# Kernel optimization log

Measured on AMD Instinct MI355X. Metric: run time of the kernel, lower is better.

## Reference

```python
import jax, jax.numpy as jnp
import numpy as np

B = 512

def conv2d(x, w, b, stride, pad):
    y = jax.lax.conv_general_dilated(x, w, (stride, stride), [(pad, pad), (pad, pad)],
                                     dimension_numbers=('NCHW', 'OIHW', 'NCHW'))
    return y + b[None, :, None, None]

def maxpool(x, k, s, pad):
    return jax.lax.reduce_window(x, -jnp.inf, jax.lax.max,
                                 (1, 1, k, k), (1, 1, s, s),
                                 [(0, 0), (0, 0), (pad, pad), (pad, pad)])

def squash(s, axis=-1):
    sq = jnp.sum(s * s, axis=axis, keepdims=True)
    return (sq / (1.0 + sq)) * s / jnp.sqrt(sq + 1e-8)

def setup_inputs() -> dict:
    key = jax.random.key(0)
    ks = jax.random.split(key, 24)
    def w(k, shape, fan_in):
        return jax.random.normal(k, shape, dtype=jnp.float32) * np.float32(np.sqrt(2.0 / fan_in))
    inp = {}
    inp['x']  = jax.random.normal(ks[0], (B, 1, 28, 28), dtype=jnp.float32)
    inp['w1'] = w(ks[1], (96, 1, 3, 3), 1 * 9);     inp['b1'] = jnp.zeros((96,), jnp.float32)
    inp['w2'] = w(ks[2], (256, 96, 3, 3), 96 * 9);  inp['b2'] = jnp.zeros((256,), jnp.float32)
    inp['w3'] = w(ks[3], (384, 256, 3, 3), 256 * 9);inp['b3'] = jnp.zeros((384,), jnp.float32)
    inp['w4'] = w(ks[4], (384, 384, 3, 3), 384 * 9);inp['b4'] = jnp.zeros((384,), jnp.float32)
    inp['w5'] = w(ks[5], (256, 384, 3, 3), 384 * 9);inp['b5'] = jnp.zeros((256,), jnp.float32)
    # PrimaryCaps conv: 256 -> 32 caps * 8 dim = 256 channels, k2 s1 p0
    inp['wp'] = w(ks[6], (256, 256, 2, 2), 256 * 4);inp['bp'] = jnp.zeros((256,), jnp.float32)
    # DenseCapsule routing weight [out_caps=10, in_caps=512, out_dim=16, in_dim=8]
    inp['Wr'] = jax.random.normal(ks[7], (10, 512, 16, 8), dtype=jnp.float32) * 0.01
    inp['fw1'] = w(ks[8], (4096, 160), 160);   inp['fb1'] = jnp.zeros((4096,), jnp.float32)
    inp['fw2'] = w(ks[9], (4096, 4096), 4096); inp['fb2'] = jnp.zeros((4096,), jnp.float32)
    inp['fw3'] = w(ks[10], (10, 4096), 4096);  inp['fb3'] = jnp.zeros((10,), jnp.float32)
    return inp

def reference(x, w1, b1, w2, b2, w3, b3, w4, b4, w5, b5, wp, bp, Wr,
              fw1, fb1, fw2, fb2, fw3, fb3):
    # AlexNet-style conv stack (eval mode; dropout = identity)
    h = jax.nn.relu(conv2d(x, w1, b1, 1, 1))   # [B,96,28,28]
    h = maxpool(h, 3, 2, 1)                    # [B,96,14,14]
    h = jax.nn.relu(conv2d(h, w2, b2, 1, 1))   # [B,256,14,14]
    h = maxpool(h, 3, 2, 1)                    # [B,256,7,7]
    h = jax.nn.relu(conv2d(h, w3, b3, 1, 1))   # [B,384,7,7]
    h = jax.nn.relu(conv2d(h, w4, b4, 1, 1))   # [B,384,7,7]
    h = jax.nn.relu(conv2d(h, w5, b5, 1, 1))   # [B,256,7,7]
    h = maxpool(h, 3, 1, 0)                    # [B,256,5,5]
    # PrimaryCaps: conv k2 -> [B,256,4,4] -> [B,512,8] -> squash
    p = conv2d(h, wp, bp, 1, 0)                # [B,256,4,4]
    u = p.reshape(p.shape[0], -1, 8)           # [B,512,8]
    u = squash(u)
    # DenseCapsule dynamic routing (3 iterations)
    x_hat = jnp.einsum('oivd,bid->boiv', Wr, u)     # [B,10,512,16]
    x_hat_d = jax.lax.stop_gradient(x_hat)
    b = jnp.zeros(x_hat.shape[:3], x_hat.dtype)     # [B,10,512]
    routings = 3
    for i in range(routings):
        c = jax.nn.softmax(b, axis=1)
        if i == routings - 1:
            v = squash(jnp.einsum('boi,boiv->bov', c, x_hat))
        else:
            v = squash(jnp.einsum('boi,boiv->bov', c, x_hat_d))
            b = b + jnp.einsum('bov,boiv->boi', v, x_hat_d)
    # Flatten + FC head
    f = v.reshape(v.shape[0], -1)                   # [B,160]
    f = jax.nn.relu(f @ fw1.T + fb1)
    f = jax.nn.relu(f @ fw2.T + fb2)
    return f @ fw3.T + fb3                          # [B,10]
```

## Files before the change

### kernel.cpp

```cpp
#include <hip/hip_runtime.h>
#include <math.h>


#define BATCH 512

typedef _Float16 half8  __attribute__((ext_vector_type(8)));
typedef _Float16 half4v __attribute__((ext_vector_type(4)));
typedef float   float4v __attribute__((ext_vector_type(4)));

__device__ __forceinline__ void gload_lds16(const void* g, void* l)
{
    __builtin_amdgcn_global_load_lds(
        (const __attribute__((address_space(1))) unsigned int*)g,
        (__attribute__((address_space(3))) unsigned int*)l,
        16, 0, 0);
}

__global__ __launch_bounds__(64) void zero_kernel(float* __restrict__ z)
{
    z[threadIdx.x] = 0.f;
}

__global__ __launch_bounds__(256) void split_kernel(
    const float* __restrict__ src, _Float16* __restrict__ hi,
    _Float16* __restrict__ lo, int n)
{
    int idx = blockIdx.x * 256 + threadIdx.x;
    if (idx >= n) return;
    float v = src[idx];
    _Float16 h = (_Float16)v;
    hi[idx] = h;
    lo[idx] = (_Float16)((v - (float)h) * 2048.0f);
}

__global__ __launch_bounds__(256) void wsplit_pad_kernel(
    const float* __restrict__ src, _Float16* __restrict__ hi,
    _Float16* __restrict__ lo, int IC, int KK, int K, int KP, int total)
{
    int idx = blockIdx.x * 256 + threadIdx.x;
    if (idx >= total) return;
    int k  = idx % KP;
    int oc = idx / KP;
    float v = 0.f;
    if (k < K) {
        int khkw = k / IC;
        int ic   = k - khkw * IC;
        v = src[((size_t)(oc * IC + ic)) * KK + khkw];
    }
    _Float16 h = (_Float16)v;
    hi[idx] = h;
    lo[idx] = (_Float16)((v - (float)h) * 2048.0f);
}

__global__ __launch_bounds__(256) void conv1_pool_nhwc(
    const float* __restrict__ x, const float* __restrict__ w1,
    const float* __restrict__ b1, _Float16* __restrict__ oh_,
    _Float16* __restrict__ ol_)
{
    int idx = blockIdx.x * 256 + threadIdx.x;
    if (idx >= 512 * 14 * 14 * 96) return;
    int oc = idx % 96; int t1 = idx / 96;
    int ow = t1 % 14;  int t2 = t1 / 14;
    int oh = t2 % 14;  int n  = t2 / 14;
    const float* xi = x + n * 784;
    float w[9];
#pragma unroll
    for (int i = 0; i < 9; ++i) w[i] = w1[oc * 9 + i];
    float bias = b1[oc];
    float best = -3.4e38f;
#pragma unroll
    for (int dy = 0; dy < 3; ++dy) {
        int ph = oh * 2 - 1 + dy;
        if ((unsigned)ph >= 28u) continue;
#pragma unroll
        for (int dx = 0; dx < 3; ++dx) {
            int pw = ow * 2 - 1 + dx;
            if ((unsigned)pw >= 28u) continue;
            float s = bias;
#pragma unroll
            for (int ky = 0; ky < 3; ++ky) {
                int iy = ph - 1 + ky;
                if ((unsigned)iy >= 28u) continue;
#pragma unroll
                for (int kx = 0; kx < 3; ++kx) {
                    int ix = pw - 1 + kx;
                    if ((unsigned)ix >= 28u) continue;
                    s = fmaf(w[ky * 3 + kx], xi[iy * 28 + ix], s);
                }
            }
            s = fmaxf(s, 0.f);
            best = fmaxf(best, s);
        }
    }
    _Float16 h = (_Float16)best;
    oh_[idx] = h;
    ol_[idx] = (_Float16)((best - (float)h) * 2048.0f);
}

template<int NB, int C, int H, int W, int OH, int OW, int KS, int STR, int PADP>
__global__ __launch_bounds__(256) void maxpool_nhwc_split(
    const float* __restrict__ in, _Float16* __restrict__ po,
    _Float16* __restrict__ pl)
{
    constexpr int TOTAL = NB * OH * OW * C;
    int idx = blockIdx.x * 256 + threadIdx.x;
    if (idx >= TOTAL) return;
    int c  = idx % C;  int t1 = idx / C;
    int ow = t1 % OW;  int t2 = t1 / OW;
    int oh = t2 % OH;  int n  = t2 / OH;
    const float* ip = in + (size_t)n * (H * W * C) + c;
    float best = -3.4e38f;
#pragma unroll
    for (int dy = 0; dy < KS; ++dy) {
        int ih = oh * STR - PADP + dy;
        if ((unsigned)ih >= (unsigned)H) continue;
#pragma unroll
        for (int dx = 0; dx < KS; ++dx) {
            int iw = ow * STR - PADP + dx;
            if ((unsigned)iw >= (unsigned)W) continue;
            best = fmaxf(best, ip[(size_t)(ih * W + iw) * C]);
        }
    }
    _Float16 h = (_Float16)best;
    po[idx] = h;
    pl[idx] = (_Float16)((best - (float)h) * 2048.0f);
}

template<int IC, int H, int W, int KH, int PAD, int OC, int NT, int OUTMODE>
__global__ __launch_bounds__(256, 2) void conv_dma(
    const _Float16* __restrict__ inh, const _Float16* __restrict__ inl,
    const _Float16* __restrict__ whi, const _Float16* __restrict__ wlo,
    const float* __restrict__ bias, const float* __restrict__ zpage,
    float* __restrict__ outf, _Float16* __restrict__ outh,
    _Float16* __restrict__ outl, int n_base)
{
    constexpr int OH  = H + 2 * PAD - KH + 1;
    constexpr int OW  = W + 2 * PAD - KH + 1;
    constexpr int OHW = OH * OW;
    constexpr int K   = IC * KH * KH;
    constexpr int KP  = (K + 63) & ~63;
    constexpr int NFRAG = NT / 32;
    constexpr int NBI   = NT / 32;
    constexpr bool UNIF = (IC % 64 == 0) && (KP == K);
    constexpr int HWIC = H * W * IC;

    const int t    = threadIdx.x;
    const int lane = t & 63;
    const int wid  = t >> 6;
    const int l15  = lane & 15;
    const int quad = lane >> 4;
    const int wm   = (wid >> 1) << 6;
    const int wn   = (wid & 1) * (NT / 2);

    const int drow  = lane >> 3;
    const int pslot = lane & 7;
    const int slog  = pslot ^ drow;

    __shared__ __align__(16) _Float16 Ah[128 * 64];
    __shared__ __align__(16) _Float16 Al[128 * 64];
    __shared__ __align__(16) _Float16 Bh[NT * 64];
    __shared__ __align__(16) _Float16 Bl[NT * 64];

    const int n0 = blockIdx.x * NT;
    const int m0 = blockIdx.y << 7;

    float4v acc1[4 * NFRAG], acc2[4 * NFRAG];
#pragma unroll
    for (int i = 0; i < 4 * NFRAG; ++i) {
        acc1[i] = (float4v)(0.f);
        acc2[i] = (float4v)(0.f);
    }

    int bU[NBI], ohU[NBI], owU[NBI];
#pragma unroll
    for (int ii = 0; ii < NBI; ++ii) {
        int nl = ((wid * NBI + ii) << 3) + drow;
        int gn = n_base + n0 + nl;
        int b  = gn / OHW;
        int p  = gn - b * OHW;
        int o  = p / OW;
        bU[ii] = b; ohU[ii] = o; owU[ii] = p - o * OW;
    }

    int khkw = 0, icb = 0;
    for (int kb = 0; kb < KP; kb += 64) {
#pragma unroll
        for (int ii = 0; ii < 4; ++ii) {
            const int iA = (wid << 2) + ii;
            const size_t go = (size_t)(m0 + (iA << 3) + drow) * KP + kb + (slog << 3);
            gload_lds16(whi + go, &Ah[(size_t)iA << 9]);
            gload_lds16(wlo + go, &Al[(size_t)iA << 9]);
        }
        if constexpr (UNIF) {
            const int kh = khkw / KH;
            const int kw = khkw - kh * KH;
#pragma unroll
            for (int ii = 0; ii < NBI; ++ii) {
                const int iB = wid * NBI + ii;
                const int ih = ohU[ii] + kh - PAD;
                const int iw = owU[ii] + kw - PAD;
                const bool ok = ((unsigned)ih < (unsigned)H) && ((unsigned)iw < (unsigned)W);
                const size_t off = (size_t)bU[ii] * HWIC + (ih * W + iw) * IC + icb + (slog << 3);
                const _Float16* sh = ok ? inh + off : (const _Float16*)zpage;
                const _Float16* sl = ok ? inl + off : (const _Float16*)zpage;
                gload_lds16(sh, &Bh[(size_t)iB << 9]);
                gload_lds16(sl, &Bl[(size_t)iB << 9]);
            }
            icb += 64;
            if (icb == IC) { icb = 0; ++khkw; }
        } else {
            const int kpl = kb + (slog << 3);
            const int kkl = kpl / IC;
            const int icl = kpl - kkl * IC;
            const int khl = kkl / KH;
            const int kwl = kkl - khl * KH;
#pragma unroll
            for (int ii = 0; ii < NBI; ++ii) {
                const int iB = wid * NBI + ii;
                const int ih = ohU[ii] + khl - PAD;
                const int iw = owU[ii] + kwl - PAD;
                const bool ok = (kpl < K) && ((unsigned)ih < (unsigned)H) &&
                                ((unsigned)iw < (unsigned)W);
                const size_t off = (size_t)bU[ii] * HWIC + (ih * W + iw) * IC + icl;
                const _Float16* sh = ok ? inh + off : (const _Float16*)zpage;
                const _Float16* sl = ok ? inl + off : (const _Float16*)zpage;
                gload_lds16(sh, &Bh[(size_t)iB << 9]);
                gload_lds16(sl, &Bl[(size_t)iB << 9]);
            }
        }
        __syncthreads();
#pragma unroll
        for (int kh2 = 0; kh2 < 2; ++kh2) {
            half8 a_h[4], a_l[4], b_h[NFRAG], b_l[NFRAG];
#pragma unroll
            for (int i = 0; i < 4; ++i) {
                const int r  = wm + (i << 4) + l15;
                const int sl = ((kh2 << 2) + quad) ^ (r & 7);
                const int off = (r << 6) + (sl << 3);
                a_h[i] = *(const half8*)&Ah[off];
                a_l[i] = *(const half8*)&Al[off];
            }
#pragma unroll
            for (int i = 0; i < NFRAG; ++i) {
                const int r  = wn + (i << 4) + l15;
                const int sl = ((kh2 << 2) + quad) ^ (r & 7);
                const int off = (r << 6) + (sl << 3);
                b_h[i] = *(const half8*)&Bh[off];
                b_l[i] = *(const half8*)&Bl[off];
            }
#pragma unroll
            for (int mi = 0; mi < 4; ++mi)
#pragma unroll
                for (int ni = 0; ni < NFRAG; ++ni) {
                    const int ix = mi * NFRAG + ni;
                    acc1[ix] = __builtin_amdgcn_mfma_f32_16x16x32_f16(a_h[mi], b_h[ni], acc1[ix], 0, 0, 0);
                    acc2[ix] = __builtin_amdgcn_mfma_f32_16x16x32_f16(a_h[mi], b_l[ni], acc2[ix], 0, 0, 0);
                    acc2[ix] = __builtin_amdgcn_mfma_f32_16x16x32_f16(a_l[mi], b_h[ni], acc2[ix], 0, 0, 0);
                }
        }
        __syncthreads();
    }
#pragma unroll
    for (int mi = 0; mi < 4; ++mi)
#pragma unroll
        for (int ni = 0; ni < NFRAG; ++ni) {
            const int ix = mi * NFRAG + ni;
            const int gn = n_base + n0 + wn + (ni << 4) + l15;
            const int ln = gn - n_base;
            const int mb = m0 + wm + (mi << 4) + (quad << 2);
            float4v bv = *(const float4v*)(bias + mb);
            float vv[4];
#pragma unroll
            for (int r = 0; r < 4; ++r) {
                float v = acc1[ix][r] + acc2[ix][r] * (1.0f / 2048.0f) + bv[r];
                if (OUTMODE != 2) v = fmaxf(v, 0.f);
                vv[r] = v;
            }
            if (OUTMODE == 0) {
                float4v o = {vv[0], vv[1], vv[2], vv[3]};
                *(float4v*)(outf + (size_t)ln * OC + mb) = o;
            } else if (OUTMODE == 1) {
                half4v hh, ll;
#pragma unroll
                for (int r = 0; r < 4; ++r) {
                    _Float16 h = (_Float16)vv[r];
                    hh[r] = h;
                    ll[r] = (_Float16)((vv[r] - (float)h) * 2048.0f);
                }
                *(half4v*)(outh + (size_t)ln * OC + mb) = hh;
                *(half4v*)(outl + (size_t)ln * OC + mb) = ll;
            } else {
                int b = gn / OHW;
                int p = gn - b * OHW;
#pragma unroll
                for (int r = 0; r < 4; ++r)
                    outf[((size_t)b * OC + mb + r) * OHW + p] = vv[r];
            }
        }
}

__global__ __launch_bounds__(256, 2) void fc2_dma(
    const _Float16* __restrict__ ah_g, const _Float16* __restrict__ al_g,
    const _Float16* __restrict__ bh_g, const _Float16* __restrict__ bl_g,
    float* __restrict__ part, int kslice)
{
    constexpr int K = 4096, N = 4096;
    const int t    = threadIdx.x;
    const int lane = t & 63;
    const int wid  = t >> 6;
    const int l15  = lane & 15;
    const int quad = lane >> 4;
    const int wm   = (wid >> 1) << 6;
    const int wn   = (wid & 1) << 6;

    const int drow  = lane >> 3;
    const int pslot = lane & 7;
    const int slog  = pslot ^ drow;

    __shared__ __align__(16) _Float16 Ah[128 * 64];
    __shared__ __align__(16) _Float16 Al[128 * 64];
    __shared__ __align__(16) _Float16 Bh[128 * 64];
    __shared__ __align__(16) _Float16 Bl[128 * 64];

    const int n0 = blockIdx.x << 7;
    const int m0 = blockIdx.y << 7;
    const int kbeg = blockIdx.z * kslice;

    float4v acc1[16], acc2[16];
#pragma unroll
    for (int i = 0; i < 16; ++i) {
        acc1[i] = (float4v)(0.f);
        acc2[i] = (float4v)(0.f);
    }

    for (int kb = 0; kb < kslice; kb += 64) {
#pragma unroll
        for (int ii = 0; ii < 4; ++ii) {
            const int iA = (wid << 2) + ii;
            const size_t ga = (size_t)(m0 + (iA << 3) + drow) * K + kbeg + kb + (slog << 3);
            gload_lds16(ah_g + ga, &Ah[(size_t)iA << 9]);
            gload_lds16(al_g + ga, &Al[(size_t)iA << 9]);
            const size_t gb = (size_t)(n0 + (iA << 3) + drow) * K + kbeg + kb + (slog << 3);
            gload_lds16(bh_g + gb, &Bh[(size_t)iA << 9]);
            gload_lds16(bl_g + gb, &Bl[(size_t)iA << 9]);
        }
        __syncthreads();
#pragma unroll
        for (int kh2 = 0; kh2 < 2; ++kh2) {
            half8 a_h[4], a_l[4], b_h[4], b_l[4];
#pragma unroll
            for (int i = 0; i < 4; ++i) {
                const int ra  = wm + (i << 4) + l15;
                const int sa  = ((kh2 << 2) + quad) ^ (ra & 7);
                const int oa  = (ra << 6) + (sa << 3);
                a_h[i] = *(const half8*)&Ah[oa];
                a_l[i] = *(const half8*)&Al[oa];
                const int rb  = wn + (i << 4) + l15;
                const int sb  = ((kh2 << 2) + quad) ^ (rb & 7);
                const int ob  = (rb << 6) + (sb << 3);
                b_h[i] = *(const half8*)&Bh[ob];
                b_l[i] = *(const half8*)&Bl[ob];
            }
#pragma unroll
            for (int mi = 0; mi < 4; ++mi)
#pragma unroll
                for (int ni = 0; ni < 4; ++ni) {
                    const int ix = mi * 4 + ni;
                    acc1[ix] = __builtin_amdgcn_mfma_f32_16x16x32_f16(a_h[mi], b_h[ni], acc1[ix], 0, 0, 0);
                    acc2[ix] = __builtin_amdgcn_mfma_f32_16x16x32_f16(a_h[mi], b_l[ni], acc2[ix], 0, 0, 0);
                    acc2[ix] = __builtin_amdgcn_mfma_f32_16x16x32_f16(a_l[mi], b_h[ni], acc2[ix], 0, 0, 0);
                }
        }
        __syncthreads();
    }
    float* po = part + (size_t)blockIdx.z * (512 * 4096);
#pragma unroll
    for (int mi = 0; mi < 4; ++mi)
#pragma unroll
        for (int ni = 0; ni < 4; ++ni) {
            const int ix = mi * 4 + ni;
            const int gn = n0 + wn + (ni << 4) + l15;
#pragma unroll
            for (int r = 0; r < 4; ++r) {
                const int m = m0 + wm + (mi << 4) + (quad << 2) + r;
                po[(size_t)m * N + gn] = acc1[ix][r] + acc2[ix][r] * (1.0f / 2048.0f);
            }
        }
}

__global__ __launch_bounds__(256) void fc2_reduce_kernel(
    const float* __restrict__ part, const float* __restrict__ bias,
    float* __restrict__ out)
{
    int idx = blockIdx.x * 256 + threadIdx.x;
    if (idx >= 512 * 4096) return;
    const size_t MN = (size_t)512 * 4096;
    float s = 0.f;
#pragma unroll
    for (int zz = 0; zz < 4; ++zz) s += part[zz * MN + idx];
    s += bias[idx & 4095];
    out[idx] = fmaxf(s, 0.f);
}

template<bool RELU>
__global__ __launch_bounds__(256) void fc_gemm(
    const float* __restrict__ A, const float* __restrict__ Bw,
    const float* __restrict__ bias, float* __restrict__ out,
    int K, int N)
{
    const int t  = threadIdx.x;
    const int j0 = blockIdx.x << 6;
    const int m0 = blockIdx.y << 7;

    __shared__ __align__(16) float As[16 * 132];
    __shared__ __align__(16) float Bs[16 * 64];

    float acc[8][4];
#pragma unroll
    for (int a = 0; a < 8; ++a)
#pragma unroll
        for (int b = 0; b < 4; ++b) acc[a][b] = 0.f;

    const int a_m  = t >> 2;
    const int a_k  = (t & 3) << 2;
    const int b_j  = t & 63;
    const int b_k0 = (t >> 6) << 2;
    const int ms = (t >> 4) << 3;
    const int js = (t & 15) << 2;

    for (int kb0 = 0; kb0 < K; kb0 += 16) {
#pragma unroll
        for (int r = 0; r < 2; ++r) {
            int m = m0 + a_m + (r << 6);
            float4 av = *(const float4*)(A + (size_t)m * K + kb0 + a_k);
            As[(a_k + 0) * 132 + a_m + (r << 6)] = av.x;
            As[(a_k + 1) * 132 + a_m + (r << 6)] = av.y;
            As[(a_k + 2) * 132 + a_m + (r << 6)] = av.z;
            As[(a_k + 3) * 132 + a_m + (r << 6)] = av.w;
        }
        {
            float4 bv = *(const float4*)(Bw + (size_t)(j0 + b_j) * K + kb0 + b_k0);
            Bs[(b_k0 + 0) * 64 + b_j] = bv.x;
            Bs[(b_k0 + 1) * 64 + b_j] = bv.y;
            Bs[(b_k0 + 2) * 64 + b_j] = bv.z;
            Bs[(b_k0 + 3) * 64 + b_j] = bv.w;
        }
        __syncthreads();
#pragma unroll
        for (int kk = 0; kk < 16; ++kk) {
            float4 A0 = *(const float4*)&As[kk * 132 + ms];
            float4 A1 = *(const float4*)&As[kk * 132 + ms + 4];
            float4 B0 = *(const float4*)&Bs[(kk << 6) + js];
            float av[8] = {A0.x, A0.y, A0.z, A0.w, A1.x, A1.y, A1.z, A1.w};
            float bv[4] = {B0.x, B0.y, B0.z, B0.w};
#pragma unroll
            for (int mm = 0; mm < 8; ++mm)
#pragma unroll
                for (int jj = 0; jj < 4; ++jj)
                    acc[mm][jj] = fmaf(av[mm], bv[jj], acc[mm][jj]);
        }
        __syncthreads();
    }
    float4 b4 = *(const float4*)(bias + j0 + js);
// ... 156 lines not shown
                    acc = fmaf(v_s[(o << 4) + v], xp[(size_t)v * (256 * 512)], acc);
                b_s[p] = acc;
            }
            __syncthreads();
        }
    }

    for (int idx = t; idx < 160; idx += 256) vout[(size_t)b * 160 + idx] = v_s[idx];
}

__global__ __launch_bounds__(256) void fc3_kernel(
    const float* __restrict__ f, const float* __restrict__ w,
    const float* __restrict__ bias, float* __restrict__ out)
{
    const int n = blockIdx.x;
    const int t = threadIdx.x;
    const int lane = t & 63, wv = t >> 6;
    const float* fr = f + (size_t)n * 4096;
    float p[10];
#pragma unroll
    for (int j = 0; j < 10; ++j) p[j] = 0.f;
    for (int k = t; k < 4096; k += 256) {
        float x = fr[k];
#pragma unroll
        for (int j = 0; j < 10; ++j) p[j] = fmaf(x, w[j * 4096 + k], p[j]);
    }
    __shared__ float red[4 * 10];
#pragma unroll
    for (int j = 0; j < 10; ++j) {
        float x = p[j];
        for (int off = 32; off > 0; off >>= 1) x += __shfl_xor(x, off);
        p[j] = x;
    }
    if (lane == 0) {
#pragma unroll
        for (int j = 0; j < 10; ++j) red[wv * 10 + j] = p[j];
    }
    __syncthreads();
    if (t < 10)
        out[(size_t)n * 10 + t] = red[t] + red[10 + t] + red[20 + t] + red[30 + t] + bias[t];
}

extern "C" void kernel_launch(void* const* d_in, const int* in_sizes, int n_in,
                              void* d_out, int out_size, void* d_ws, size_t ws_size,
                              hipStream_t stream)
{
    const float* x   = (const float*)d_in[0];
    const float* w1  = (const float*)d_in[1];
    const float* b1  = (const float*)d_in[2];
    const float* w2  = (const float*)d_in[3];
    const float* b2  = (const float*)d_in[4];
    const float* w3  = (const float*)d_in[5];
    const float* b3  = (const float*)d_in[6];
    const float* w4  = (const float*)d_in[7];
    const float* b4  = (const float*)d_in[8];
    const float* w5  = (const float*)d_in[9];
    const float* b5  = (const float*)d_in[10];
    const float* wp  = (const float*)d_in[11];
    const float* bp  = (const float*)d_in[12];
    const float* Wr  = (const float*)d_in[13];
    const float* fw1 = (const float*)d_in[14];
    const float* fb1 = (const float*)d_in[15];
    const float* fw2 = (const float*)d_in[16];
    const float* fb2 = (const float*)d_in[17];
    const float* fw3 = (const float*)d_in[18];
    const float* fb3 = (const float*)d_in[19];
    float* outp = (float*)d_out;

    char* w = (char*)d_ws;
    _Float16* w2h  = (_Float16*)(w + 115605504);
    _Float16* w2l  = (_Float16*)(w + 116064256);
    _Float16* w3h  = (_Float16*)(w + 116523008);
    _Float16* w3l  = (_Float16*)(w + 118292480);
    _Float16* w4h  = (_Float16*)(w + 120061952);
    _Float16* w4l  = (_Float16*)(w + 122716160);
    _Float16* w5h  = (_Float16*)(w + 125370368);
    _Float16* w5l  = (_Float16*)(w + 127139840);
    _Float16* wph  = (_Float16*)(w + 128909312);
    _Float16* wpl  = (_Float16*)(w + 129433600);
    float*    zp   = (float*)(w + 129957888);

    _Float16* p1h  = (_Float16*)(w + 0);
    _Float16* p1l  = (_Float16*)(w + 19267584);
    float*    a2   = (float*)(w + 38535168);
    _Float16* p2h  = (_Float16*)(w + 89915392);
    _Float16* p2l  = (_Float16*)(w + 102760448);
    _Float16* a3h  = (_Float16*)(w + 0);
    _Float16* a3l  = (_Float16*)(w + 19267584);
    _Float16* a4h  = (_Float16*)(w + 38535168);
    _Float16* a4l  = (_Float16*)(w + 57802752);
    float*    a5   = (float*)(w + 0);
    _Float16* p3h  = (_Float16*)(w + 25690112);
    _Float16* p3l  = (_Float16*)(w + 32243712);
    float*    pc   = (float*)(w + 0);
    float*    u    = (float*)(w + 8388608);
    float*    vcap = (float*)(w + 16777216);
    float*    xh   = (float*)(w + 17104896);

    float*    f1   = (float*)(w + 17104896);
    _Float16* fw2h = (_Float16*)(w + 33882112);
    _Float16* fw2l = (_Float16*)(w + 67436544);
    _Float16* f1h  = (_Float16*)(w + 100990976);
    _Float16* f1l  = (_Float16*)(w + 105185280);
    float*    part = (float*)(w + 0);
    float*    f2   = (float*)(w + 33882112);

    zero_kernel<<<dim3(1), dim3(64), 0, stream>>>(zp);
    wsplit_pad_kernel<<<dim3(896),  dim3(256), 0, stream>>>(w2, w2h, w2l,  96, 9,  864,  896,  229376);
    wsplit_pad_kernel<<<dim3(3456), dim3(256), 0, stream>>>(w3, w3h, w3l, 256, 9, 2304, 2304,  884736);
    wsplit_pad_kernel<<<dim3(5184), dim3(256), 0, stream>>>(w4, w4h, w4l, 384, 9, 3456, 3456, 1327104);
    wsplit_pad_kernel<<<dim3(3456), dim3(256), 0, stream>>>(w5, w5h, w5l, 384, 9, 3456, 3456,  884736);
    wsplit_pad_kernel<<<dim3(1024), dim3(256), 0, stream>>>(wp, wph, wpl, 256, 4, 1024, 1024,  262144);

    conv1_pool_nhwc<<<dim3(37632), dim3(256), 0, stream>>>(x, w1, b1, p1h, p1l);

    conv_dma<96, 14, 14, 3, 1, 256, 128, 0><<<dim3(392, 2), dim3(256), 0, stream>>>(
        p1h, p1l, w2h, w2l, b2, zp, a2, nullptr, nullptr, 0);
    maxpool_nhwc_split<256, 256, 14, 14, 7, 7, 3, 2, 1><<<dim3(12544), dim3(256), 0, stream>>>(
        a2, p2h, p2l);
    conv_dma<96, 14, 14, 3, 1, 256, 128, 0><<<dim3(392, 2), dim3(256), 0, stream>>>(
        p1h, p1l, w2h, w2l, b2, zp, a2, nullptr, nullptr, 50176);
    maxpool_nhwc_split<256, 256, 14, 14, 7, 7, 3, 2, 1><<<dim3(12544), dim3(256), 0, stream>>>(
        a2, p2h + (size_t)3211264, p2l + (size_t)3211264);

    conv_dma<256, 7, 7, 3, 1, 384, 128, 1><<<dim3(196, 3), dim3(256), 0, stream>>>(
        p2h, p2l, w3h, w3l, b3, zp, nullptr, a3h, a3l, 0);
    conv_dma<384, 7, 7, 3, 1, 384, 128, 1><<<dim3(196, 3), dim3(256), 0, stream>>>(
        a3h, a3l, w4h, w4l, b4, zp, nullptr, a4h, a4l, 0);
    conv_dma<384, 7, 7, 3, 1, 256, 128, 0><<<dim3(196, 2), dim3(256), 0, stream>>>(
        a4h, a4l, w5h, w5l, b5, zp, a5, nullptr, nullptr, 0);
    maxpool_nhwc_split<512, 256, 7, 7, 5, 5, 3, 1, 0><<<dim3(12800), dim3(256), 0, stream>>>(
        a5, p3h, p3l);
    conv_dma<256, 5, 5, 2, 0, 256, 64, 2><<<dim3(128, 2), dim3(256), 0, stream>>>(
        p3h, p3l, wph, wpl, bp, zp, pc, nullptr, nullptr, 0);
    squash_kernel<<<dim3(1024), dim3(256), 0, stream>>>(pc, u);

    for (int h = 0; h < 2; ++h) {
        const float* uh = u + (size_t)h * 256 * 4096;
        float* vh = vcap + (size_t)h * 256 * 160;
        xhat_kernel<<<dim3(16, 10), dim3(256), 0, stream>>>(uh, Wr, xh);
        routing2_kernel<<<dim3(256), dim3(256), 0, stream>>>(xh, vh);
    }

    split_kernel<<<dim3(65536), dim3(256), 0, stream>>>(fw2, fw2h, fw2l, 16777216);

    fc_gemm<true><<<dim3(64, 4), dim3(256), 0, stream>>>(vcap, fw1, fb1, f1, 160, 4096);
    split_kernel<<<dim3(8192), dim3(256), 0, stream>>>(f1, f1h, f1l, 2097152);
    fc2_dma<<<dim3(32, 4, 4), dim3(256), 0, stream>>>(f1h, f1l, fw2h, fw2l, part, 1024);
    fc2_reduce_kernel<<<dim3(8192), dim3(256), 0, stream>>>(part, fb2, f2);
    fc3_kernel<<<dim3(512), dim3(256), 0, stream>>>(f2, fw3, fb3, outp);
}
```

Measured before the change: 1.403 ms.

## Double-buffer LDS in conv and FC2 GEMMs with 8-wave blocks

Rewrites the conv and FC2 GEMM kernels so they double-buffer the LDS tiles. The next K-slice's global-to-LDS DMA loads are issued before computing on the current slice, gated by explicit vmcnt waits and raw s_barrier. Blocks grow from 4 to 8 waves, with per-wave N work halved, and MFMA sections are bracketed with s_setprio. The goal is to overlap memory latency with MFMA work. The cost is doubled LDS per block, which likely allows only one block per CU and reduces scheduling flexibility.

```diff
diff --git a/kernel.cpp b/kernel.cpp
--- a/kernel.cpp
+++ b/kernel.cpp
@@ -14,6 +14,14 @@
         (const __attribute__((address_space(1))) unsigned int*)g,
         (__attribute__((address_space(3))) unsigned int*)l,
         16, 0, 0);
+}
+
+template<int N> __device__ __forceinline__ void waitcnt_vm()
+{
+    static_assert(N == 0 || N == 6 || N == 8, "unsupported vmcnt");
+    if constexpr (N == 8)      asm volatile("s_waitcnt vmcnt(8)" ::: "memory");
+    else if constexpr (N == 6) asm volatile("s_waitcnt vmcnt(6)" ::: "memory");
+    else                       asm volatile("s_waitcnt vmcnt(0)" ::: "memory");
 }
 
 __global__ __launch_bounds__(64) void zero_kernel(float* __restrict__ z)
@@ -127,7 +135,7 @@
 }
 
 template<int IC, int H, int W, int KH, int PAD, int OC, int NT, int OUTMODE>
-__global__ __launch_bounds__(256, 2) void conv_dma(
+__global__ __launch_bounds__(512, 2) void conv_pipe(
     const _Float16* __restrict__ inh, const _Float16* __restrict__ inl,
     const _Float16* __restrict__ whi, const _Float16* __restrict__ wlo,
     const float* __restrict__ bias, const float* __restrict__ zpage,
@@ -139,8 +147,9 @@
     constexpr int OHW = OH * OW;
     constexpr int K   = IC * KH * KH;
     constexpr int KP  = (K + 63) & ~63;
-    constexpr int NFRAG = NT / 32;
-    constexpr int NBI   = NT / 32;
+    constexpr int NFRAG = NT / 64;
+    constexpr int NBI   = NT / 64;
+    constexpr int VMC   = 4 + 2 * NBI;
     constexpr bool UNIF = (IC % 64 == 0) && (KP == K);
     constexpr int HWIC = H * W * IC;
 
@@ -149,17 +158,17 @@
     const int wid  = t >> 6;
     const int l15  = lane & 15;
     const int quad = lane >> 4;
-    const int wm   = (wid >> 1) << 6;
-    const int wn   = (wid & 1) * (NT / 2);
+    const int wm   = (wid >> 2) << 6;
+    const int wn   = (wid & 3) * (NT / 4);
 
     const int drow  = lane >> 3;
     const int pslot = lane & 7;
     const int slog  = pslot ^ drow;
 
-    __shared__ __align__(16) _Float16 Ah[128 * 64];
-    __shared__ __align__(16) _Float16 Al[128 * 64];
-    __shared__ __align__(16) _Float16 Bh[NT * 64];
-    __shared__ __align__(16) _Float16 Bl[NT * 64];
+    __shared__ __align__(16) _Float16 AhS[2][128 * 64];
+    __shared__ __align__(16) _Float16 AlS[2][128 * 64];
+    __shared__ __align__(16) _Float16 BhS[2][NT * 64];
+    __shared__ __align__(16) _Float16 BlS[2][NT * 64];
 
     const int n0 = blockIdx.x * NT;
     const int m0 = blockIdx.y << 7;
@@ -182,16 +191,17 @@
         bU[ii] = b; ohU[ii] = o; owU[ii] = p - o * OW;
     }
 
-    int khkw = 0, icb = 0;
-    for (int kb = 0; kb < KP; kb += 64) {
-#pragma unroll
-        for (int ii = 0; ii < 4; ++ii) {
-            const int iA = (wid << 2) + ii;
-            const size_t go = (size_t)(m0 + (iA << 3) + drow) * KP + kb + (slog << 3);
-            gload_lds16(whi + go, &Ah[(size_t)iA << 9]);
-            gload_lds16(wlo + go, &Al[(size_t)iA << 9]);
+    auto STAGE = [&](int buf, int kb_s) {
+#pragma unroll
+        for (int ii = 0; ii < 2; ++ii) {
+            const int iA = (wid << 1) + ii;
+            const size_t go = (size_t)(m0 + (iA << 3) + drow) * KP + kb_s + (slog << 3);
+            gload_lds16(whi + go, &AhS[buf][iA << 9]);
+            gload_lds16(wlo + go, &AlS[buf][iA << 9]);
         }
         if constexpr (UNIF) {
+            const int khkw = kb_s / IC;
+            const int icb  = kb_s - khkw * IC;
             const int kh = khkw / KH;
             const int kw = khkw - kh * KH;
 #pragma unroll
@@ -201,15 +211,11 @@
                 const int iw = owU[ii] + kw - PAD;
                 const bool ok = ((unsigned)ih < (unsigned)H) && ((unsigned)iw < (unsigned)W);
                 const size_t off = (size_t)bU[ii] * HWIC + (ih * W + iw) * IC + icb + (slog << 3);
-                const _Float16* sh = ok ? inh + off : (const _Float16*)zpage;
-                const _Float16* sl = ok ? inl + off : (const _Float16*)zpage;
-                gload_lds16(sh, &Bh[(size_t)iB << 9]);
-                gload_lds16(sl, &Bl[(size_t)iB << 9]);
-            }
-            icb += 64;
-            if (icb == IC) { icb = 0; ++khkw; }
+                gload_lds16(ok ? inh + off : (const _Float16*)zpage, &BhS[buf][iB << 9]);
+                gload_lds16(ok ? inl + off : (const _Float16*)zpage, &BlS[buf][iB << 9]);
+            }
         } else {
-            const int kpl = kb + (slog << 3);
+            const int kpl = kb_s + (slog << 3);
             const int kkl = kpl / IC;
             const int icl = kpl - kkl * IC;
             const int khl = kkl / KH;
@@ -222,13 +228,17 @@
                 const bool ok = (kpl < K) && ((unsigned)ih < (unsigned)H) &&
                                 ((unsigned)iw < (unsigned)W);
                 const size_t off = (size_t)bU[ii] * HWIC + (ih * W + iw) * IC + icl;
-                const _Float16* sh = ok ? inh + off : (const _Float16*)zpage;
-                const _Float16* sl = ok ? inl + off : (const _Float16*)zpage;
-                gload_lds16(sh, &Bh[(size_t)iB << 9]);
-                gload_lds16(sl, &Bl[(size_t)iB << 9]);
-            }
-        }
-        __syncthreads();
+                gload_lds16(ok ? inh + off : (const _Float16*)zpage, &BhS[buf][iB << 9]);
+                gload_lds16(ok ? inl + off : (const _Float16*)zpage, &BlS[buf][iB << 9]);
+            }
+        }
+    };
+
+    auto COMPUTE = [&](int buf) {
+        const _Float16* Ahb = &AhS[buf][0];
+        const _Float16* Alb = &AlS[buf][0];
+        const _Float16* Bhb = &BhS[buf][0];
+        const _Float16* Blb = &BlS[buf][0];
 #pragma unroll
         for (int kh2 = 0; kh2 < 2; ++kh2) {
             half8 a_h[4], a_l[4], b_h[NFRAG], b_l[NFRAG];
@@ -237,17 +247,18 @@
                 const int r  = wm + (i << 4) + l15;
                 const int sl = ((kh2 << 2) + quad) ^ (r & 7);
                 const int off = (r << 6) + (sl << 3);
-                a_h[i] = *(const half8*)&Ah[off];
-                a_l[i] = *(const half8*)&Al[off];
+                a_h[i] = *(const half8*)&Ahb[off];
+                a_l[i] = *(const half8*)&Alb[off];
             }
 #pragma unroll
             for (int i = 0; i < NFRAG; ++i) {
                 const int r  = wn + (i << 4) + l15;
                 const int sl = ((kh2 << 2) + quad) ^ (r & 7);
                 const int off = (r << 6) + (sl << 3);
-                b_h[i] = *(const half8*)&Bh[off];
-                b_l[i] = *(const half8*)&Bl[off];
-            }
+                b_h[i] = *(const half8*)&Bhb[off];
+                b_l[i] = *(const half8*)&Blb[off];
+            }
+            __builtin_amdgcn_s_setprio(1);
 #pragma unroll
             for (int mi = 0; mi < 4; ++mi)
 #pragma unroll
@@ -257,9 +268,28 @@
                     acc2[ix] = __builtin_amdgcn_mfma_f32_16x16x32_f16(a_h[mi], b_l[ni], acc2[ix], 0, 0, 0);
                     acc2[ix] = __builtin_amdgcn_mfma_f32_16x16x32_f16(a_l[mi], b_h[ni], acc2[ix], 0, 0, 0);
                 }
-        }
-        __syncthreads();
-    }
+            __builtin_amdgcn_s_setprio(0);
+        }
+    };
+
+    STAGE(0, 0);
+    int cur = 0;
+#pragma unroll 1
+    for (int kb = 0; kb + 64 < KP; kb += 64) {
+        STAGE(cur ^ 1, kb + 64);
+        waitcnt_vm<VMC>();
+        __builtin_amdgcn_s_barrier();
+        __builtin_amdgcn_sched_barrier(0);
+        COMPUTE(cur);
+        __builtin_amdgcn_sched_barrier(0);
+        __builtin_amdgcn_s_barrier();
+        cur ^= 1;
+    }
+    waitcnt_vm<0>();
+    __builtin_amdgcn_s_barrier();
+    __builtin_amdgcn_sched_barrier(0);
+    COMPUTE(cur);
+
 #pragma unroll
     for (int mi = 0; mi < 4; ++mi)
 #pragma unroll
@@ -299,7 +329,7 @@
         }
 }
 
-__global__ __launch_bounds__(256, 2) void fc2_dma(
+__global__ __launch_bounds__(512, 2) void fc2_pipe(
     const _Float16* __restrict__ ah_g, const _Float16* __restrict__ al_g,
     const _Float16* __restrict__ bh_g, const _Float16* __restrict__ bl_g,
     float* __restrict__ part, int kslice)
@@ -310,75 +340,104 @@
     const int wid  = t >> 6;
     const int l15  = lane & 15;
     const int quad = lane >> 4;
-    const int wm   = (wid >> 1) << 6;
-    const int wn   = (wid & 1) << 6;
+    const int wm   = (wid >> 2) << 6;
+    const int wn   = (wid & 3) << 5;
 
     const int drow  = lane >> 3;
     const int pslot = lane & 7;
     const int slog  = pslot ^ drow;
 
-    __shared__ __align__(16) _Float16 Ah[128 * 64];
-    __shared__ __align__(16) _Float16 Al[128 * 64];
-    __shared__ __align__(16) _Float16 Bh[128 * 64];
-    __shared__ __align__(16) _Float16 Bl[128 * 64];
+    __shared__ __align__(16) _Float16 AhS[2][128 * 64];
+    __shared__ __align__(16) _Float16 AlS[2][128 * 64];
+    __shared__ __align__(16) _Float16 BhS[2][128 * 64];
+    __shared__ __align__(16) _Float16 BlS[2][128 * 64];
 
     const int n0 = blockIdx.x << 7;
     const int m0 = blockIdx.y << 7;
     const int kbeg = blockIdx.z * kslice;
 
-    float4v acc1[16], acc2[16];
-#pragma unroll
-    for (int i = 0; i < 16; ++i) {
+    float4v acc1[8], acc2[8];
+#pragma unroll
+    for (int i = 0; i < 8; ++i) {
         acc1[i] = (float4v)(0.f);
         acc2[i] = (float4v)(0.f);
     }
 
-    for (int kb = 0; kb < kslice; kb += 64) {
-#pragma unroll
-        for (int ii = 0; ii < 4; ++ii) {
-            const int iA = (wid << 2) + ii;
-            const size_t ga = (size_t)(m0 + (iA << 3) + drow) * K + kbeg + kb + (slog << 3);
-            gload_lds16(ah_g + ga, &Ah[(size_t)iA << 9]);
-            gload_lds16(al_g + ga, &Al[(size_t)iA << 9]);
-            const size_t gb = (size_t)(n0 + (iA << 3) + drow) * K + kbeg + kb + (slog << 3);
-            gload_lds16(bh_g + gb, &Bh[(size_t)iA << 9]);
-            gload_lds16(bl_g + gb, &Bl[(size_t)iA << 9]);
-        }
-        __syncthreads();
+    auto STAGE = [&](int buf, int kb_s) {
+#pragma unroll
+        for (int ii = 0; ii < 2; ++ii) {
+            const int iA = (wid << 1) + ii;
+            const size_t ga = (size_t)(m0 + (iA << 3) + drow) * K + kbeg + kb_s + (slog << 3);
+            gload_lds16(ah_g + ga, &AhS[buf][iA << 9]);
+            gload_lds16(al_g + ga, &AlS[buf][iA << 9]);
+            const size_t gb = (size_t)(n0 + (iA << 3) + drow) * K + kbeg + kb_s + (slog << 3);
+            gload_lds16(bh_g + gb, &BhS[buf][iA << 9]);
+            gload_lds16(bl_g + gb, &BlS[buf][iA << 9]);
+        }
+    };
+
+    auto COMPUTE = [&](int buf) {
+        const _Float16* Ahb = &AhS[buf][0];
+        const _Float16* Alb = &AlS[buf][0];
+        const _Float16* Bhb = &BhS[buf][0];
+        const _Float16* Blb = &BlS[buf][0];
 #pragma unroll
         for (int kh2 = 0; kh2 < 2; ++kh2) {
-            half8 a_h[4], a_l[4], b_h[4], b_l[4];
+            half8 a_h[4], a_l[4], b_h[2], b_l[2];
 #pragma unroll
             for (int i = 0; i < 4; ++i) {
-                const int ra  = wm + (i << 4) + l15;
-                const int sa  = ((kh2 << 2) + quad) ^ (ra & 7);
-                const int oa  = (ra << 6) + (sa << 3);
-                a_h[i] = *(const half8*)&Ah[oa];
-                a_l[i] = *(const half8*)&Al[oa];
-                const int rb  = wn + (i << 4) + l15;
-                const int sb  = ((kh2 << 2) + quad) ^ (rb & 7);
-                const int ob  = (rb << 6) + (sb << 3);
-                b_h[i] = *(const half8*)&Bh[ob];
-                b_l[i] = *(const half8*)&Bl[ob];
-            }
+                const int r  = wm + (i << 4) + l15;
+                const int sl = ((kh2 << 2) + quad) ^ (r & 7);
+                const int off = (r << 6) + (sl << 3);
+                a_h[i] = *(const half8*)&Ahb[off];
+                a_l[i] = *(const half8*)&Alb[off];
+            }
+#pragma unroll
+            for (int i = 0; i < 2; ++i) {
+                const int r  = wn + (i << 4) + l15;
+                const int sl = ((kh2 << 2) + quad) ^ (r & 7);
+                const int off = (r << 6) + (sl << 3);
+                b_h[i] = *(const half8*)&Bhb[off];
+                b_l[i] = *(const half8*)&Blb[off];
+            }
+            __builtin_amdgcn_s_setprio(1);
 #pragma unroll
             for (int mi = 0; mi < 4; ++mi)
 #pragma unroll
-                for (int ni = 0; ni < 4; ++ni) {
-                    const int ix = mi * 4 + ni;
+                for (int ni = 0; ni < 2; ++ni) {
+                    const int ix = (mi << 1) + ni;
                     acc1[ix] = __builtin_amdgcn_mfma_f32_16x16x32_f16(a_h[mi], b_h[ni], acc1[ix], 0, 0, 0);
                     acc2[ix] = __builtin_amdgcn_mfma_f32_16x16x32_f16(a_h[mi], b_l[ni], acc2[ix], 0, 0, 0);
                     acc2[ix] = __builtin_amdgcn_mfma_f32_16x16x32_f16(a_l[mi], b_h[ni], acc2[ix], 0, 0, 0);
                 }
-        }
-        __syncthreads();
-    }
+            __builtin_amdgcn_s_setprio(0);
+        }
+    };
+
+    STAGE(0, 0);
+    int cur = 0;
+#pragma unroll 1
+    for (int kb = 0; kb + 64 < kslice; kb += 64) {
+        STAGE(cur ^ 1, kb + 64);
+        waitcnt_vm<8>();
+        __builtin_amdgcn_s_barrier();
+        __builtin_amdgcn_sched_barrier(0);
+        COMPUTE(cur);
+        __builtin_amdgcn_sched_barrier(0);
+        __builtin_amdgcn_s_barrier();
+        cur ^= 1;
+    }
+    waitcnt_vm<0>();
+    __builtin_amdgcn_s_barrier();
+    __builtin_amdgcn_sched_barrier(0);
+    COMPUTE(cur);
+
     float* po = part + (size_t)blockIdx.z * (512 * 4096);
 #pragma unroll
     for (int mi = 0; mi < 4; ++mi)
 #pragma unroll
-        for (int ni = 0; ni < 4; ++ni) {
-            const int ix = mi * 4 + ni;
+        for (int ni = 0; ni < 2; ++ni) {
+            const int ix = (mi << 1) + ni;
             const int gn = n0 + wn + (ni << 4) + l15;
 #pragma unroll
             for (int r = 0; r < 4; ++r) {
@@ -733,24 +792,24 @@
 
     conv1_pool_nhwc<<<dim3(37632), dim3(256), 0, stream>>>(x, w1, b1, p1h, p1l);
 
-    conv_dma<96, 14, 14, 3, 1, 256, 128, 0><<<dim3(392, 2), dim3(256), 0, stream>>>(
+    conv_pipe<96, 14, 14, 3, 1, 256, 128, 0><<<dim3(392, 2), dim3(512), 0, stream>>>(
         p1h, p1l, w2h, w2l, b2, zp, a2, nullptr, nullptr, 0);
     maxpool_nhwc_split<256, 256, 14, 14, 7, 7, 3, 2, 1><<<dim3(12544), dim3(256), 0, stream>>>(
         a2, p2h, p2l);
-    conv_dma<96, 14, 14, 3, 1, 256, 128, 0><<<dim3(392, 2), dim3(256), 0, stream>>>(
+    conv_pipe<96, 14, 14, 3, 1, 256, 128, 0><<<dim3(392, 2), dim3(512), 0, stream>>>(
         p1h, p1l, w2h, w2l, b2, zp, a2, nullptr, nullptr, 50176);
     maxpool_nhwc_split<256, 256, 14, 14, 7, 7, 3, 2, 1><<<dim3(12544), dim3(256), 0, stream>>>(
         a2, p2h + (size_t)3211264, p2l + (size_t)3211264);
 
-    conv_dma<256, 7, 7, 3, 1, 384, 128, 1><<<dim3(196, 3), dim3(256), 0, stream>>>(
+    conv_pipe<256, 7, 7, 3, 1, 384, 128, 1><<<dim3(196, 3), dim3(512), 0, stream>>>(
         p2h, p2l, w3h, w3l, b3, zp, nullptr, a3h, a3l, 0);
-    conv_dma<384, 7, 7, 3, 1, 384, 128, 1><<<dim3(196, 3), dim3(256), 0, stream>>>(
+    conv_pipe<384, 7, 7, 3, 1, 384, 128, 1><<<dim3(196, 3), dim3(512), 0, stream>>>(
         a3h, a3l, w4h, w4l, b4, zp, nullptr, a4h, a4l, 0);
-    conv_dma<384, 7, 7, 3, 1, 256, 128, 0><<<dim3(196, 2), dim3(256), 0, stream>>>(
+    conv_pipe<384, 7, 7, 3, 1, 256, 128, 0><<<dim3(196, 2), dim3(512), 0, stream>>>(
         a4h, a4l, w5h, w5l, b5, zp, a5, nullptr, nullptr, 0);
     maxpool_nhwc_split<512, 256, 7, 7, 5, 5, 3, 1, 0><<<dim3(12800), dim3(256), 0, stream>>>(
         a5, p3h, p3l);
-    conv_dma<256, 5, 5, 2, 0, 256, 64, 2><<<dim3(128, 2), dim3(256), 0, stream>>>(
+    conv_pipe<256, 5, 5, 2, 0, 256, 64, 2><<<dim3(128, 2), dim3(512), 0, stream>>>(
         p3h, p3l, wph, wpl, bp, zp, pc, nullptr, nullptr, 0);
     squash_kernel<<<dim3(1024), dim3(256), 0, stream>>>(pc, u);
 
@@ -765,7 +824,7 @@
 
     fc_gemm<true><<<dim3(64, 4), dim3(256), 0, stream>>>(vcap, fw1, fb1, f1, 160, 4096);
     split_kernel<<<dim3(8192), dim3(256), 0, stream>>>(f1, f1h, f1l, 2097152);
-    fc2_dma<<<dim3(32, 4, 4), dim3(256), 0, stream>>>(f1h, f1l, fw2h, fw2l, part, 1024);
+    fc2_pipe<<<dim3(32, 4, 4), dim3(512), 0, stream>>>(f1h, f1l, fw2h, fw2l, part, 1024);
     fc2_reduce_kernel<<<dim3(8192), dim3(256), 0, stream>>>(part, fb2, f2);
     fc3_kernel<<<dim3(512), dim3(256), 0, stream>>>(f2, fw3, fb3, outp);
 }
```

Result: slower. 1.788 ms (+27.4%).

## Store conv activations as split fp16 pairs and remap blocks across XCDs

Applied to the files above, without the earlier changes.

Conv2 and conv5 now write their outputs as hi/lo fp16 pairs (OUTMODE 1) instead of fp32, and the maxpool kernels read those pairs back, rebuild the value, and re-split it. Activation traffic stays the same size but the pool no longer has to convert from fp32. The conv launches now use a 1D grid with an XCD-aware mapping of block id to (n, m) tile, so tiles that share data are placed on the same XCD for better L2 reuse. The split pair adds a small rounding step on those intermediates.

```diff
diff --git a/kernel.cpp b/kernel.cpp
--- a/kernel.cpp
+++ b/kernel.cpp
@@ -98,9 +98,9 @@
 }
 
 template<int NB, int C, int H, int W, int OH, int OW, int KS, int STR, int PADP>
-__global__ __launch_bounds__(256) void maxpool_nhwc_split(
-    const float* __restrict__ in, _Float16* __restrict__ po,
-    _Float16* __restrict__ pl)
+__global__ __launch_bounds__(256) void maxpool_resplit(
+    const _Float16* __restrict__ ih_, const _Float16* __restrict__ il_,
+    _Float16* __restrict__ po, _Float16* __restrict__ pl)
 {
     constexpr int TOTAL = NB * OH * OW * C;
     int idx = blockIdx.x * 256 + threadIdx.x;
@@ -108,17 +108,19 @@
     int c  = idx % C;  int t1 = idx / C;
     int ow = t1 % OW;  int t2 = t1 / OW;
     int oh = t2 % OH;  int n  = t2 / OH;
-    const float* ip = in + (size_t)n * (H * W * C) + c;
+    const size_t base = (size_t)n * (H * W * C) + c;
     float best = -3.4e38f;
 #pragma unroll
     for (int dy = 0; dy < KS; ++dy) {
-        int ih = oh * STR - PADP + dy;
-        if ((unsigned)ih >= (unsigned)H) continue;
+        int ihh = oh * STR - PADP + dy;
+        if ((unsigned)ihh >= (unsigned)H) continue;
 #pragma unroll
         for (int dx = 0; dx < KS; ++dx) {
-            int iw = ow * STR - PADP + dx;
-            if ((unsigned)iw >= (unsigned)W) continue;
-            best = fmaxf(best, ip[(size_t)(ih * W + iw) * C]);
+            int iww = ow * STR - PADP + dx;
+            if ((unsigned)iww >= (unsigned)W) continue;
+            const size_t off = base + (size_t)(ihh * W + iww) * C;
+            float v = (float)ih_[off] + (float)il_[off] * (1.0f / 2048.0f);
+            best = fmaxf(best, v);
         }
     }
     _Float16 h = (_Float16)best;
@@ -126,7 +128,7 @@
     pl[idx] = (_Float16)((best - (float)h) * 2048.0f);
 }
 
-template<int IC, int H, int W, int KH, int PAD, int OC, int NT, int OUTMODE>
+template<int IC, int H, int W, int KH, int PAD, int OC, int NT, int NBN, int OUTMODE>
 __global__ __launch_bounds__(256, 2) void conv_dma(
     const _Float16* __restrict__ inh, const _Float16* __restrict__ inl,
     const _Float16* __restrict__ whi, const _Float16* __restrict__ wlo,
@@ -143,6 +145,8 @@
     constexpr int NBI   = NT / 32;
     constexpr bool UNIF = (IC % 64 == 0) && (KP == K);
     constexpr int HWIC = H * W * IC;
+    constexpr int MB   = OC >> 7;
+    constexpr int NWG  = NBN * MB;
 
     const int t    = threadIdx.x;
     const int lane = t & 63;
@@ -161,8 +165,13 @@
     __shared__ __align__(16) _Float16 Bh[NT * 64];
     __shared__ __align__(16) _Float16 Bl[NT * 64];
 
-    const int n0 = blockIdx.x * NT;
-    const int m0 = blockIdx.y << 7;
+    const int bid = blockIdx.x;
+    constexpr int q = NWG >> 3, rr = NWG & 7;
+    const int xcd = bid & 7, boff = bid >> 3;
+    const int lg = (xcd < rr) ? (xcd * (q + 1) + boff)
+                              : (rr * (q + 1) + (xcd - rr) * q + boff);
+    const int n0 = (lg % NBN) * NT;
+    const int m0 = (lg / NBN) << 7;
 
     float4v acc1[4 * NFRAG], acc2[4 * NFRAG];
 #pragma unroll
@@ -701,14 +710,16 @@
 
     _Float16* p1h  = (_Float16*)(w + 0);
     _Float16* p1l  = (_Float16*)(w + 19267584);
-    float*    a2   = (float*)(w + 38535168);
+    _Float16* a2h  = (_Float16*)(w + 38535168);
+    _Float16* a2l  = (_Float16*)(w + 64225280);
     _Float16* p2h  = (_Float16*)(w + 89915392);
     _Float16* p2l  = (_Float16*)(w + 102760448);
     _Float16* a3h  = (_Float16*)(w + 0);
     _Float16* a3l  = (_Float16*)(w + 19267584);
     _Float16* a4h  = (_Float16*)(w + 38535168);
     _Float16* a4l  = (_Float16*)(w + 57802752);
-    float*    a5   = (float*)(w + 0);
+    _Float16* a5h  = (_Float16*)(w + 0);
+    _Float16* a5l  = (_Float16*)(w + 12845056);
     _Float16* p3h  = (_Float16*)(w + 25690112);
     _Float16* p3l  = (_Float16*)(w + 32243712);
     float*    pc   = (float*)(w + 0);
@@ -733,24 +744,24 @@
 
     conv1_pool_nhwc<<<dim3(37632), dim3(256), 0, stream>>>(x, w1, b1, p1h, p1l);
 
-    conv_dma<96, 14, 14, 3, 1, 256, 128, 0><<<dim3(392, 2), dim3(256), 0, stream>>>(
-        p1h, p1l, w2h, w2l, b2, zp, a2, nullptr, nullptr, 0);
-    maxpool_nhwc_split<256, 256, 14, 14, 7, 7, 3, 2, 1><<<dim3(12544), dim3(256), 0, stream>>>(
-        a2, p2h, p2l);
-    conv_dma<96, 14, 14, 3, 1, 256, 128, 0><<<dim3(392, 2), dim3(256), 0, stream>>>(
-        p1h, p1l, w2h, w2l, b2, zp, a2, nullptr, nullptr, 50176);
-    maxpool_nhwc_split<256, 256, 14, 14, 7, 7, 3, 2, 1><<<dim3(12544), dim3(256), 0, stream>>>(
-        a2, p2h + (size_t)3211264, p2l + (size_t)3211264);
-
-    conv_dma<256, 7, 7, 3, 1, 384, 128, 1><<<dim3(196, 3), dim3(256), 0, stream>>>(
+    conv_dma<96, 14, 14, 3, 1, 256, 128, 392, 1><<<dim3(784), dim3(256), 0, stream>>>(
+        p1h, p1l, w2h, w2l, b2, zp, nullptr, a2h, a2l, 0);
+    maxpool_resplit<256, 256, 14, 14, 7, 7, 3, 2, 1><<<dim3(12544), dim3(256), 0, stream>>>(
+        a2h, a2l, p2h, p2l);
+    conv_dma<96, 14, 14, 3, 1, 256, 128, 392, 1><<<dim3(784), dim3(256), 0, stream>>>(
+        p1h, p1l, w2h, w2l, b2, zp, nullptr, a2h, a2l, 50176);
+    maxpool_resplit<256, 256, 14, 14, 7, 7, 3, 2, 1><<<dim3(12544), dim3(256), 0, stream>>>(
+        a2h, a2l, p2h + (size_t)3211264, p2l + (size_t)3211264);
+
+    conv_dma<256, 7, 7, 3, 1, 384, 128, 196, 1><<<dim3(588), dim3(256), 0, stream>>>(
         p2h, p2l, w3h, w3l, b3, zp, nullptr, a3h, a3l, 0);
-    conv_dma<384, 7, 7, 3, 1, 384, 128, 1><<<dim3(196, 3), dim3(256), 0, stream>>>(
+    conv_dma<384, 7, 7, 3, 1, 384, 128, 196, 1><<<dim3(588), dim3(256), 0, stream>>>(
         a3h, a3l, w4h, w4l, b4, zp, nullptr, a4h, a4l, 0);
-    conv_dma<384, 7, 7, 3, 1, 256, 128, 0><<<dim3(196, 2), dim3(256), 0, stream>>>(
-        a4h, a4l, w5h, w5l, b5, zp, a5, nullptr, nullptr, 0);
-    maxpool_nhwc_split<512, 256, 7, 7, 5, 5, 3, 1, 0><<<dim3(12800), dim3(256), 0, stream>>>(
-        a5, p3h, p3l);
-    conv_dma<256, 5, 5, 2, 0, 256, 64, 2><<<dim3(128, 2), dim3(256), 0, stream>>>(
+    conv_dma<384, 7, 7, 3, 1, 256, 128, 196, 1><<<dim3(392), dim3(256), 0, stream>>>(
+        a4h, a4l, w5h, w5l, b5, zp, nullptr, a5h, a5l, 0);
+    maxpool_resplit<512, 256, 7, 7, 5, 5, 3, 1, 0><<<dim3(12800), dim3(256), 0, stream>>>(
+        a5h, a5l, p3h, p3l);
+    conv_dma<256, 5, 5, 2, 0, 256, 64, 128, 2><<<dim3(256), dim3(256), 0, stream>>>(
         p3h, p3l, wph, wpl, bp, zp, pc, nullptr, nullptr, 0);
     squash_kernel<<<dim3(1024), dim3(256), 0, stream>>>(pc, u);
 
```

Result: slower. 1.444 ms (+2.9%).

## Split-K conv3 and conv4 into two slices with a combine kernel

Applied to the files above, without the earlier changes.

Adds a split-K template parameter to conv_dma so conv3 and conv4 run with two K slices along gridDim.z. Each slice writes partial sums as hi/lo fp16 pairs, and a new combine kernel adds the pairs, applies bias and ReLU, and re-splits the result. The aim is to double the block count (588 to 1176) so the GPU's CUs are better filled. In exchange it adds extra partial-buffer traffic, one more launch per layer, and some precision loss from storing partials in the split fp16 format.

```diff
diff --git a/kernel.cpp b/kernel.cpp
--- a/kernel.cpp
+++ b/kernel.cpp
@@ -126,7 +126,7 @@
     pl[idx] = (_Float16)((best - (float)h) * 2048.0f);
 }
 
-template<int IC, int H, int W, int KH, int PAD, int OC, int NT, int OUTMODE>
+template<int IC, int H, int W, int KH, int PAD, int OC, int NT, int ZS, int OUTMODE>
 __global__ __launch_bounds__(256, 2) void conv_dma(
     const _Float16* __restrict__ inh, const _Float16* __restrict__ inl,
     const _Float16* __restrict__ whi, const _Float16* __restrict__ wlo,
@@ -139,6 +139,8 @@
     constexpr int OHW = OH * OW;
     constexpr int K   = IC * KH * KH;
     constexpr int KP  = (K + 63) & ~63;
+    constexpr int KSL = KP / ZS;
+    static_assert(KSL % 64 == 0, "slice must be K-step aligned");
     constexpr int NFRAG = NT / 32;
     constexpr int NBI   = NT / 32;
     constexpr bool UNIF = (IC % 64 == 0) && (KP == K);
@@ -163,6 +165,7 @@
 
     const int n0 = blockIdx.x * NT;
     const int m0 = blockIdx.y << 7;
+    const int kbeg = blockIdx.z * KSL;
 
     float4v acc1[4 * NFRAG], acc2[4 * NFRAG];
 #pragma unroll
@@ -182,8 +185,9 @@
         bU[ii] = b; ohU[ii] = o; owU[ii] = p - o * OW;
     }
 
-    int khkw = 0, icb = 0;
-    for (int kb = 0; kb < KP; kb += 64) {
+    int khkw = kbeg / IC;
+    int icb  = kbeg - khkw * IC;
+    for (int kb = kbeg; kb < kbeg + KSL; kb += 64) {
 #pragma unroll
         for (int ii = 0; ii < 4; ++ii) {
             const int iA = (wid << 2) + ii;
@@ -260,6 +264,7 @@
         }
         __syncthreads();
     }
+    const size_t zoff = (size_t)blockIdx.z * ((size_t)gridDim.x * NT * OC * 2);
 #pragma unroll
     for (int mi = 0; mi < 4; ++mi)
 #pragma unroll
@@ -268,18 +273,20 @@
             const int gn = n_base + n0 + wn + (ni << 4) + l15;
             const int ln = gn - n_base;
             const int mb = m0 + wm + (mi << 4) + (quad << 2);
-            float4v bv = *(const float4v*)(bias + mb);
+            float4v bv;
+            if constexpr (OUTMODE != 4) bv = *(const float4v*)(bias + mb);
+            else                        bv = (float4v)(0.f);
             float vv[4];
 #pragma unroll
             for (int r = 0; r < 4; ++r) {
                 float v = acc1[ix][r] + acc2[ix][r] * (1.0f / 2048.0f) + bv[r];
-                if (OUTMODE != 2) v = fmaxf(v, 0.f);
+                if (OUTMODE != 2 && OUTMODE != 4) v = fmaxf(v, 0.f);
                 vv[r] = v;
             }
             if (OUTMODE == 0) {
                 float4v o = {vv[0], vv[1], vv[2], vv[3]};
                 *(float4v*)(outf + (size_t)ln * OC + mb) = o;
-            } else if (OUTMODE == 1) {
+            } else if (OUTMODE == 1 || OUTMODE == 4) {
                 half4v hh, ll;
 #pragma unroll
                 for (int r = 0; r < 4; ++r) {
@@ -287,8 +294,8 @@
                     hh[r] = h;
                     ll[r] = (_Float16)((vv[r] - (float)h) * 2048.0f);
                 }
-                *(half4v*)(outh + (size_t)ln * OC + mb) = hh;
-                *(half4v*)(outl + (size_t)ln * OC + mb) = ll;
+                *(half4v*)(outh + zoff + (size_t)ln * OC + mb) = hh;
+                *(half4v*)(outl + zoff + (size_t)ln * OC + mb) = ll;
             } else {
                 int b = gn / OHW;
                 int p = gn - b * OHW;
@@ -297,6 +304,34 @@
                     outf[((size_t)b * OC + mb + r) * OHW + p] = vv[r];
             }
         }
+}
+
+__global__ __launch_bounds__(256) void conv_combine2(
+    const _Float16* __restrict__ p0h, const _Float16* __restrict__ p0l,
+    const float* __restrict__ bias, _Float16* __restrict__ oh,
+    _Float16* __restrict__ ol, int total8, int OC, size_t zoff)
+{
+    int t8 = blockIdx.x * 256 + threadIdx.x;
+    if (t8 >= total8) return;
+    size_t base = (size_t)t8 * 8;
+    half8 ah = *(const half8*)(p0h + base);
+    half8 al = *(const half8*)(p0l + base);
+    half8 bh = *(const half8*)(p0h + zoff + base);
+    half8 bl = *(const half8*)(p0l + zoff + base);
+    int oc0 = (int)(base % (size_t)OC);
+    half8 hh, ll;
+#pragma unroll
+    for (int j = 0; j < 8; ++j) {
+        float v = (float)ah[j] + (float)al[j] * (1.0f / 2048.0f)
+                + (float)bh[j] + (float)bl[j] * (1.0f / 2048.0f)
+                + bias[oc0 + j];
+        v = fmaxf(v, 0.f);
+        _Float16 h = (_Float16)v;
+        hh[j] = h;
+        ll[j] = (_Float16)((v - (float)h) * 2048.0f);
+    }
+    *(half8*)(oh + base) = hh;
+    *(half8*)(ol + base) = ll;
 }
 
 __global__ __launch_bounds__(256, 2) void fc2_dma(
@@ -704,10 +739,13 @@
     float*    a2   = (float*)(w + 38535168);
     _Float16* p2h  = (_Float16*)(w + 89915392);
     _Float16* p2l  = (_Float16*)(w + 102760448);
-    _Float16* a3h  = (_Float16*)(w + 0);
-    _Float16* a3l  = (_Float16*)(w + 19267584);
-    _Float16* a4h  = (_Float16*)(w + 38535168);
-    _Float16* a4l  = (_Float16*)(w + 57802752);
+
+    _Float16* cp0h = (_Float16*)(w + 0);
+    _Float16* cp0l = (_Float16*)(w + 19267584);
+    _Float16* a3h  = (_Float16*)(w + 77070336);
+    _Float16* a3l  = (_Float16*)(w + 96337920);
+    _Float16* a4h  = (_Float16*)(w + 77070336);
+    _Float16* a4l  = (_Float16*)(w + 96337920);
     float*    a5   = (float*)(w + 0);
     _Float16* p3h  = (_Float16*)(w + 25690112);
     _Float16* p3l  = (_Float16*)(w + 32243712);
@@ -733,24 +771,28 @@
 
     conv1_pool_nhwc<<<dim3(37632), dim3(256), 0, stream>>>(x, w1, b1, p1h, p1l);
 
-    conv_dma<96, 14, 14, 3, 1, 256, 128, 0><<<dim3(392, 2), dim3(256), 0, stream>>>(
+    conv_dma<96, 14, 14, 3, 1, 256, 128, 1, 0><<<dim3(392, 2), dim3(256), 0, stream>>>(
         p1h, p1l, w2h, w2l, b2, zp, a2, nullptr, nullptr, 0);
     maxpool_nhwc_split<256, 256, 14, 14, 7, 7, 3, 2, 1><<<dim3(12544), dim3(256), 0, stream>>>(
         a2, p2h, p2l);
-    conv_dma<96, 14, 14, 3, 1, 256, 128, 0><<<dim3(392, 2), dim3(256), 0, stream>>>(
+    conv_dma<96, 14, 14, 3, 1, 256, 128, 1, 0><<<dim3(392, 2), dim3(256), 0, stream>>>(
         p1h, p1l, w2h, w2l, b2, zp, a2, nullptr, nullptr, 50176);
     maxpool_nhwc_split<256, 256, 14, 14, 7, 7, 3, 2, 1><<<dim3(12544), dim3(256), 0, stream>>>(
         a2, p2h + (size_t)3211264, p2l + (size_t)3211264);
 
-    conv_dma<256, 7, 7, 3, 1, 384, 128, 1><<<dim3(196, 3), dim3(256), 0, stream>>>(
-        p2h, p2l, w3h, w3l, b3, zp, nullptr, a3h, a3l, 0);
-    conv_dma<384, 7, 7, 3, 1, 384, 128, 1><<<dim3(196, 3), dim3(256), 0, stream>>>(
-        a3h, a3l, w4h, w4l, b4, zp, nullptr, a4h, a4l, 0);
-    conv_dma<384, 7, 7, 3, 1, 256, 128, 0><<<dim3(196, 2), dim3(256), 0, stream>>>(
+    conv_dma<256, 7, 7, 3, 1, 384, 128, 2, 4><<<dim3(196, 3, 2), dim3(256), 0, stream>>>(
+        p2h, p2l, w3h, w3l, b3, zp, nullptr, cp0h, cp0l, 0);
+    conv_combine2<<<dim3(4704), dim3(256), 0, stream>>>(
+        cp0h, cp0l, b3, a3h, a3l, 1204224, 384, (size_t)19267584);
+    conv_dma<384, 7, 7, 3, 1, 384, 128, 2, 4><<<dim3(196, 3, 2), dim3(256), 0, stream>>>(
+        a3h, a3l, w4h, w4l, b4, zp, nullptr, cp0h, cp0l, 0);
+    conv_combine2<<<dim3(4704), dim3(256), 0, stream>>>(
+        cp0h, cp0l, b4, a4h, a4l, 1204224, 384, (size_t)19267584);
+    conv_dma<384, 7, 7, 3, 1, 256, 128, 1, 0><<<dim3(196, 2), dim3(256), 0, stream>>>(
         a4h, a4l, w5h, w5l, b5, zp, a5, nullptr, nullptr, 0);
     maxpool_nhwc_split<512, 256, 7, 7, 5, 5, 3, 1, 0><<<dim3(12800), dim3(256), 0, stream>>>(
         a5, p3h, p3l);
-    conv_dma<256, 5, 5, 2, 0, 256, 64, 2><<<dim3(128, 2), dim3(256), 0, stream>>>(
+    conv_dma<256, 5, 5, 2, 0, 256, 64, 1, 2><<<dim3(128, 2), dim3(256), 0, stream>>>(
         p3h, p3l, wph, wpl, bp, zp, pc, nullptr, nullptr, 0);
     squash_kernel<<<dim3(1024), dim3(256), 0, stream>>>(pc, u);
 
```

Result: no change. 1.385 ms (-1.3%).
